# Kernel tuning notes

Measured on AMD Instinct MI355X. Metric: run time of the kernel, lower is better.

Reference implementation:

```python
import jax, jax.numpy as jnp
import numpy as np

COND_EPS = 1e-12  # singularity threshold for the 2x2 Hessian determinant


def setup_inputs() -> dict:
    key = jax.random.key(0)
    k1, k2 = jax.random.split(key)
    b, h, w = 8, 1024, 1536
    # neur_beta_eme: non-negative-ish network output (forward clamps at 0 anyway)
    neur_beta_eme = jax.random.uniform(k1, (b, 1, h, w), dtype=jnp.float32) * 2.0
    base_detector_score = jax.random.normal(k2, (b, 1, h, w), dtype=jnp.float32)
    return {
        "neur_beta_eme": neur_beta_eme,
        "base_detector_score": base_detector_score,
        "n": 2048,
        "border_size": 16,
    }


def _gather(score_flat, y, x, w):
    # score_flat: [b, h*w]; y,x: [b,n] -> [b,n]
    return jnp.take_along_axis(score_flat, y * w + x, axis=-1)


def reference(neur_beta_eme, base_detector_score, n, border_size):
    b, _, h, w = base_detector_score.shape
    # NeSSDetector.forward: model(image)[-1].clamp(min=0)
    neur = jnp.maximum(neur_beta_eme, 0.0)
    score = base_detector_score

    # base_detector.get_extrema_mask: 3x3 NMS (local max) + border exclusion
    pooled = jax.lax.reduce_window(score, -jnp.inf, jax.lax.max,
                                   (1, 1, 3, 3), (1, 1, 1, 1), "SAME")
    ys = jnp.arange(h)
    xs = jnp.arange(w)
    border = (((ys >= border_size) & (ys < h - border_size))[:, None]
              & ((xs >= border_size) & (xs < w - border_size))[None, :])
    extrema_mask = (score == pooled) & border[None, None]

    # ness_extrema_map = exp(-neur_beta_eme) * extrema_mask
    ness = jnp.exp(-neur) * extrema_mask.astype(score.dtype)

    # topk over flattened spatial dims
    ness_flat = ness.reshape(b, -1)                      # [b, h*w]
    _, flat_cand_kp = jax.lax.top_k(ness_flat, n)        # [b, n]

    # flat2grid(flat, w) + 0.5  (pixel-center coords, (y, x) order)
    y = flat_cand_kp // w
    x = flat_cand_kp % w
    cand_kp = jnp.stack([y, x], axis=-1).astype(score.dtype) + 0.5  # [b, n, 2]

    # localize_keypoints_via_taylor: 3x3 finite-difference gradient/Hessian,
    # solve H @ inc = -g per keypoint (2x2 closed-form solve)
    sf = score.reshape(b, -1)
    yc = jnp.clip(y, 1, h - 2)
    xc = jnp.clip(x, 1, w - 2)
    s00 = _gather(sf, yc, xc, w)
    sp0 = _gather(sf, yc + 1, xc, w)
    sm0 = _gather(sf, yc - 1, xc, w)
    s0p = _gather(sf, yc, xc + 1, w)
    s0m = _gather(sf, yc, xc - 1, w)
    spp = _gather(sf, yc + 1, xc + 1, w)
    spm = _gather(sf, yc + 1, xc - 1, w)
    smp = _gather(sf, yc - 1, xc + 1, w)
    smm = _gather(sf, yc - 1, xc - 1, w)

    gy = 0.5 * (sp0 - sm0)
    gx = 0.5 * (s0p - s0m)
    hyy = sp0 - 2.0 * s00 + sm0
    hxx = s0p - 2.0 * s00 + s0m
    hxy = 0.25 * (spp - spm - smp + smm)

    det = hyy * hxx - hxy * hxy
    sing_mask = jnp.abs(det) > COND_EPS
    safe_det = jnp.where(sing_mask, det, 1.0)
    inc_y = -(hxx * gy - hxy * gx) / safe_det
    inc_x = -(hyy * gx - hxy * gy) / safe_det
    inc = jnp.stack([inc_y, inc_x], axis=-1)             # [b, n, 2]
    inc = jnp.clip(jnp.where(sing_mask[..., None], inc, 0.0), -0.5, 0.5)

    kp = cand_kp + inc                                   # [b, n, 2]

    # kp_neur_beta_eme = neur.view(b,-1).gather(-1, flat_cand_kp)
    kp_neur = jnp.take_along_axis(neur.reshape(b, -1), flat_cand_kp, axis=-1)

    return jnp.concatenate([kp, kp_neur[..., None]], axis=-1)  # [b, n, 3]
```

## Files before the change

kernel.cpp:

```cpp
#include <hip/hip_runtime.h>
#include <math.h>

typedef unsigned int u32;
typedef unsigned long long u64;

#define B 8
#define H 1024
#define W 1536
#define NPIX (H * W)
#define NK 2048
#define BORDER 16
#define NSEG 64
#define TY 8
#define NTILE 6
#define GRIDY 31
#define HBINS 512
#define TOPK_CAP 4096
#define SEG_CAP_MAX 4096
#define CTR_PAD 32
#define IDX_MASK 0x1FFFFFu

#define OFF_TCOUNT 128
#define OFF_HIST   4096
#define OFF_SEGCNT 20480
#define OFF_RANK   86016
#define OFF_KEYS   217088
#define OFF_CAND   479232

__global__ __launch_bounds__(256) void cand_k(const float* __restrict__ neur,
                                              const float* __restrict__ score,
                                              u32* __restrict__ candp,
                                              u32* __restrict__ segcnt,
                                              u32* __restrict__ hist, int seg_cap) {
    __shared__ u32 lh[HBINS];
    int tile = blockIdx.x;
    int b = blockIdx.z;
    int wave = threadIdx.x >> 6;
    int lane = threadIdx.x & 63;
    for (int i = threadIdx.x; i < HBINS; i += 256) lh[i] = 0;
    __syncthreads();

    int strip = blockIdx.y * 4 + wave;
    int y0 = BORDER + strip * TY;
    int x0 = tile * 256 + lane * 4;
    const float* s = score + (size_t)b * NPIX;
    const float* nb = neur + (size_t)b * NPIX;
    bool haveL = (tile > 0) && (lane == 0);
    bool haveR = (tile < NTILE - 1) && (lane == 63);

    float4 rv[TY + 2];
    float4 nvv[TY];
    float le[TY + 2], re[TY + 2];
    const float* base_row = s + (size_t)(y0 - 1) * W + x0;
    const float* nrow = nb + (size_t)y0 * W + x0;
    #pragma unroll
    for (int r = 0; r < TY + 2; ++r) rv[r] = *(const float4*)(base_row + (size_t)r * W);
    #pragma unroll
    for (int r = 0; r < TY; ++r) nvv[r] = *(const float4*)(nrow + (size_t)r * W);
    #pragma unroll
    for (int r = 0; r < TY + 2; ++r) {
        le[r] = haveL ? base_row[(size_t)r * W - 1] : 0.0f;
        re[r] = haveR ? base_row[(size_t)r * W + 4] : 0.0f;
    }

    bool xok[4];
    #pragma unroll
    for (int e = 0; e < 4; ++e) {
        int x = x0 + e;
        xok[e] = (x >= BORDER) && (x < W - BORDER);
    }

    u32 extbits = 0;
    {
        float4 hm, h0, hp;
        #pragma unroll
        for (int r = 0; r < 2; ++r) {
            float4 c = rv[r];
            float l = __shfl_up(c.w, 1); if (haveL) l = le[r];
            float rr = __shfl_down(c.x, 1); if (haveR) rr = re[r];
            float4 hh;
            hh.x = fmaxf(fmaxf(l, c.x), c.y);
            hh.y = fmaxf(fmaxf(c.x, c.y), c.z);
            hh.z = fmaxf(fmaxf(c.y, c.z), c.w);
            hh.w = fmaxf(fmaxf(c.z, c.w), rr);
            if (r == 0) hm = hh; else h0 = hh;
        }
        #pragma unroll
        for (int ys = 0; ys < TY; ++ys) {
            float4 c = rv[ys + 2];
            float l = __shfl_up(c.w, 1); if (haveL) l = le[ys + 2];
            float rr = __shfl_down(c.x, 1); if (haveR) rr = re[ys + 2];
            hp.x = fmaxf(fmaxf(l, c.x), c.y);
            hp.y = fmaxf(fmaxf(c.x, c.y), c.z);
            hp.z = fmaxf(fmaxf(c.y, c.z), c.w);
            hp.w = fmaxf(fmaxf(c.z, c.w), rr);
            float pv[4];
            pv[0] = fmaxf(fmaxf(hm.x, h0.x), hp.x);
            pv[1] = fmaxf(fmaxf(hm.y, h0.y), hp.y);
            pv[2] = fmaxf(fmaxf(hm.z, h0.z), hp.z);
            pv[3] = fmaxf(fmaxf(hm.w, h0.w), hp.w);
            float4 c0 = rv[ys + 1];
            float cv[4] = {c0.x, c0.y, c0.z, c0.w};
            #pragma unroll
            for (int e = 0; e < 4; ++e)
                if (xok[e] && cv[e] >= pv[e]) extbits |= (1u << (ys * 4 + e));
            hm = h0; h0 = hp;
        }
    }

    u32 c = (u32)__popc(extbits);
    u32 scan = c;
    #pragma unroll
    for (int off = 1; off < 64; off <<= 1) {
        u32 o = (u32)__shfl_up((int)scan, off, 64);
        if (lane >= off) scan += o;
    }
    u32 excl = scan - c;
    u32 tot = (u32)__shfl((int)scan, 63, 64);
    if (tot) {
        int seg = (strip * NTILE + tile) & (NSEG - 1);
        u32* ctr = &segcnt[(u32)(b * NSEG + seg) * CTR_PAD];
        u32 base = 0;
        if (lane == 63) base = atomicAdd(ctr, scan);
        base = (u32)__shfl((int)base, 63, 64);
        u32 pos0 = base + excl;
        u32 sbase = (u32)(b * NSEG + seg) * (u32)seg_cap;
        u32 idxbase = (u32)(y0 * W + x0);
        #pragma unroll
        for (int k = 0; k < 32; ++k) {
            if (extbits & (1u << k)) {
                const int ro = k >> 2, e = k & 3;
                float4 nq = nvv[ro];
                float raw = (e == 0) ? nq.x : (e == 1) ? nq.y : (e == 2) ? nq.z : nq.w;
                float nv = fmaxf(raw, 0.0f);
                u32 fb = __float_as_uint(nv);
                u32 bin = fb >> 21; if (bin > HBINS - 1) bin = HBINS - 1;
                atomicAdd(&lh[bin], 1u);
                u32 idx = idxbase + (u32)ro * W + (u32)e;
                u32 p = pos0 + (u32)__popc(extbits & ((1u << k) - 1u));
                if ((int)p < seg_cap) candp[sbase + p] = (bin << 21) | idx;
            }
        }
    }
    __syncthreads();
    for (int i = threadIdx.x; i < HBINS; i += 256) {
        u32 v = lh[i];
        if (v) atomicAdd(&hist[(u32)b * HBINS + i], v);
    }
}

__global__ __launch_bounds__(256) void compact_k(const u32* __restrict__ candp,
                                                 const u32* __restrict__ segcnt,
                                                 const u32* __restrict__ hist,
                                                 const float* __restrict__ neur,
                                                 u64* __restrict__ keysout,
                                                 u32* tcount, int seg_cap) {
    __shared__ u32 piv_s;
    int seg = blockIdx.x;
    int b = blockIdx.y;
    int lane = threadIdx.x & 63;
    if (threadIdx.x < 64) {
        if (threadIdx.x == 0) piv_s = 0xFFFFFFFFu;
        u32 v[8];
        u32 s8 = 0;
        #pragma unroll
        for (int e = 0; e < 8; ++e) {
            v[e] = hist[(u32)b * HBINS + (u32)threadIdx.x * 8u + e];
            s8 += v[e];
        }
        u32 incl = s8;
        #pragma unroll
        for (int off = 1; off < 64; off <<= 1) {
            u32 o = (u32)__shfl_up((int)incl, off, 64);
            if (lane >= off) incl += o;
        }
        u32 excl = incl - s8;
        if (excl < NK && incl >= NK) {
            u32 cum = excl;
            u32 T = 0;
            #pragma unroll
            for (int e = 0; e < 8; ++e) {
                cum += v[e];
                if (cum >= NK) { T = (u32)threadIdx.x * 8u + e; break; }
            }
            piv_s = (T + 2u) << 21;
        }
    }
    __syncthreads();
    u32 piv = piv_s;
    const float* nb = neur + (size_t)b * NPIX;

    u32 cnt = segcnt[(u32)(b * NSEG + seg) * CTR_PAD];
    if ((int)cnt > seg_cap) cnt = (u32)seg_cap;
    u32 base = (u32)(b * NSEG + seg) * (u32)seg_cap;
    u32 iters = (cnt + 255u) / 256u;
    for (u32 it = 0; it < iters; ++it) {
        u32 i = it * 256u + threadIdx.x;
        bool f = false;
        u32 idx = 0;
        if (i < cnt) {
            u32 p = candp[base + i];
            f = (p < piv);
            idx = p & IDX_MASK;
        }
        u64 m = __ballot((int)f);
        if (m) {
            int leader = __ffsll((long long)m) - 1;
            u32 wbase = 0;
            if (lane == leader) wbase = atomicAdd(&tcount[b * CTR_PAD], (u32)__popcll(m));
            wbase = (u32)__shfl((int)wbase, leader, 64);
            if (f) {
                u32 pos = wbase + (u32)__popcll(m & ((1ull << (u32)lane) - 1ull));
                if (pos < TOPK_CAP) {
                    float nv = fmaxf(nb[idx], 0.0f);
                    float ness = (float)exp(-(double)nv);
                    keysout[(u32)b * TOPK_CAP + pos] =
                        ((u64)__float_as_uint(ness) << 32) | (u32)(~idx);
                }
            }
        }
    }
}

__global__ __launch_bounds__(1024) void rank_k(const u64* __restrict__ keys,
                                               u32* __restrict__ rank) {
    __shared__ u64 jk[1024];
    int b = blockIdx.z;
    u32 i = blockIdx.x * 1024u + threadIdx.x;
    u64 ki = keys[(u32)b * TOPK_CAP + i];
    jk[threadIdx.x] = keys[(u32)b * TOPK_CAP + blockIdx.y * 1024u + threadIdx.x];
    __syncthreads();
    u32 r = 0;
    #pragma unroll 8
    for (int j = 0; j < 1024; ++j) r += (jk[j] > ki) ? 1u : 0u;
    if (r) atomicAdd(&rank[(u32)b * TOPK_CAP + i], r);
}

__global__ __launch_bounds__(256) void refine_k(const float* __restrict__ neur,
                                                const float* __restrict__ score,
                                                const u64* __restrict__ keys,
                                                const u32* __restrict__ rank,
                                                float* __restrict__ out) {
    int b = blockIdx.y;
    u32 i = blockIdx.x * 256u + threadIdx.x;
    u32 r = rank[(u32)b * TOPK_CAP + i];
    if (r >= NK) return;
    const float* s = score + (size_t)b * NPIX;
    const float* nb = neur + (size_t)b * NPIX;
    u64 key = keys[(u32)b * TOPK_CAP + i];
    u32 idx = ~(u32)key;
    if (idx >= (u32)NPIX) return;
    int y = (int)(idx / W), x = (int)(idx % W);
    int yc = min(max(y, 1), H - 2), xc = min(max(x, 1), W - 2);
    int p = yc * W + xc;
    float s00 = s[p], sp0 = s[p + W], sm0 = s[p - W], s0p = s[p + 1], s0m = s[p - 1];
    float spp = s[p + W + 1], spm = s[p + W - 1], smp = s[p - W + 1], smm = s[p - W - 1];
    float gy = 0.5f * (sp0 - sm0);
    float gx = 0.5f * (s0p - s0m);
    float hyy = sp0 - 2.0f * s00 + sm0;
    float hxx = s0p - 2.0f * s00 + s0m;
    float hxy = 0.25f * (spp - spm - smp + smm);
    float det = hyy * hxx - hxy * hxy;
    bool sing = fabsf(det) > 1e-12f;
    float sd = sing ? det : 1.0f;
    float iy = -(hxx * gy - hxy * gx) / sd;
    float ix = -(hyy * gx - hxy * gy) / sd;
    if (!sing) { iy = 0.0f; ix = 0.0f; }
    iy = fminf(fmaxf(iy, -0.5f), 0.5f);
    ix = fminf(fmaxf(ix, -0.5f), 0.5f);
    size_t o = ((size_t)b * NK + (size_t)r) * 3;
    out[o] = (float)y + 0.5f + iy;
    out[o + 1] = (float)x + 0.5f + ix;
    out[o + 2] = fmaxf(nb[idx], 0.0f);
}

extern "C" void kernel_launch(void* const* d_in, const int* in_sizes, int n_in,
                              void* d_out, int out_size, void* d_ws, size_t ws_size,
                              hipStream_t stream) {
    const float* neur = (const float*)d_in[0];
    const float* score = (const float*)d_in[1];
    float* out = (float*)d_out;
    char* ws = (char*)d_ws;
    u32* tcount = (u32*)(ws + OFF_TCOUNT);
    u32* hist = (u32*)(ws + OFF_HIST);
    u32* segcnt = (u32*)(ws + OFF_SEGCNT);
    u32* rank = (u32*)(ws + OFF_RANK);
    u64* keysbuf = (u64*)(ws + OFF_KEYS);
    u32* candp = (u32*)(ws + OFF_CAND);

    size_t avail = ws_size > OFF_CAND ? ws_size - OFF_CAND : 0;
    long long cap_ll = (long long)(avail / (4ull * B * NSEG));
    int seg_cap = cap_ll > SEG_CAP_MAX ? SEG_CAP_MAX : (int)cap_ll;

    hipMemsetAsync(ws, 0, OFF_CAND, stream);
    cand_k<<<dim3(NTILE, GRIDY, B), 256, 0, stream>>>(neur, score, candp, segcnt, hist, seg_cap);
    compact_k<<<dim3(NSEG, B), 256, 0, stream>>>(candp, segcnt, hist, neur, keysbuf, tcount, seg_cap);
    rank_k<<<dim3(TOPK_CAP / 1024, TOPK_CAP / 1024, B), 1024, 0, stream>>>(keysbuf, rank);
    refine_k<<<dim3(TOPK_CAP / 256, B), 256, 0, stream>>>(neur, score, keysbuf, rank, out);
}
```

Before: 178.7 us.

## Fuse rank and refine kernels, load all keys to LDS, drop rank memset

Merges the separate rank-counting and refinement kernels into a single kernel. Each block loads the batch's full key array (masked by the valid count) into shared memory and computes each key's rank directly, so the global rank buffer, its atomics and part of the workspace memset are no longer needed. Removing one launch and the rank buffer traffic is the main aim. In exchange each block now scans 4096 keys instead of 1024, the grid shrinks from 128 blocks of 1024 threads to 128 blocks of 256 threads, and each block needs 32KB of LDS, which reduces parallelism for the rank computation.

```diff
diff --git a/kernel.cpp b/kernel.cpp
--- a/kernel.cpp
+++ b/kernel.cpp
@@ -23,9 +23,9 @@
 #define OFF_TCOUNT 128
 #define OFF_HIST   4096
 #define OFF_SEGCNT 20480
-#define OFF_RANK   86016
-#define OFF_KEYS   217088
-#define OFF_CAND   479232
+#define OFF_ZERO_END 86016
+#define OFF_KEYS   86016
+#define OFF_CAND   348160
 
 __global__ __launch_bounds__(256) void cand_k(const float* __restrict__ neur,
                                               const float* __restrict__ score,
@@ -222,34 +222,30 @@
     }
 }
 
-__global__ __launch_bounds__(1024) void rank_k(const u64* __restrict__ keys,
-                                               u32* __restrict__ rank) {
-    __shared__ u64 jk[1024];
-    int b = blockIdx.z;
-    u32 i = blockIdx.x * 1024u + threadIdx.x;
-    u64 ki = keys[(u32)b * TOPK_CAP + i];
-    jk[threadIdx.x] = keys[(u32)b * TOPK_CAP + blockIdx.y * 1024u + threadIdx.x];
-    __syncthreads();
+__global__ __launch_bounds__(256) void rankref_k(const float* __restrict__ neur,
+                                                 const float* __restrict__ score,
+                                                 const u64* __restrict__ keys,
+                                                 const u32* __restrict__ tcount,
+                                                 float* __restrict__ out) {
+    __shared__ u64 jk[TOPK_CAP];
+    int b = blockIdx.y;
+    u32 cnt = tcount[(u32)b * CTR_PAD];
+    if (cnt > TOPK_CAP) cnt = TOPK_CAP;
+    for (u32 t = threadIdx.x; t < TOPK_CAP; t += 256u)
+        jk[t] = (t < cnt) ? keys[(u32)b * TOPK_CAP + t] : 0ull;
+    __syncthreads();
+
+    u32 i = blockIdx.x * 256u + threadIdx.x;
+    u64 ki = jk[i];
     u32 r = 0;
-    #pragma unroll 8
-    for (int j = 0; j < 1024; ++j) r += (jk[j] > ki) ? 1u : 0u;
-    if (r) atomicAdd(&rank[(u32)b * TOPK_CAP + i], r);
-}
-
-__global__ __launch_bounds__(256) void refine_k(const float* __restrict__ neur,
-                                                const float* __restrict__ score,
-                                                const u64* __restrict__ keys,
-                                                const u32* __restrict__ rank,
-                                                float* __restrict__ out) {
-    int b = blockIdx.y;
-    u32 i = blockIdx.x * 256u + threadIdx.x;
-    u32 r = rank[(u32)b * TOPK_CAP + i];
-    if (r >= NK) return;
+    #pragma unroll 16
+    for (int j = 0; j < TOPK_CAP; ++j) r += (jk[j] > ki) ? 1u : 0u;
+    if (i >= cnt || r >= NK) return;
+
+    u32 idx = ~(u32)ki;
+    if (idx >= (u32)NPIX) return;
     const float* s = score + (size_t)b * NPIX;
     const float* nb = neur + (size_t)b * NPIX;
-    u64 key = keys[(u32)b * TOPK_CAP + i];
-    u32 idx = ~(u32)key;
-    if (idx >= (u32)NPIX) return;
     int y = (int)(idx / W), x = (int)(idx % W);
     int yc = min(max(y, 1), H - 2), xc = min(max(x, 1), W - 2);
     int p = yc * W + xc;
@@ -284,7 +280,6 @@
     u32* tcount = (u32*)(ws + OFF_TCOUNT);
     u32* hist = (u32*)(ws + OFF_HIST);
     u32* segcnt = (u32*)(ws + OFF_SEGCNT);
-    u32* rank = (u32*)(ws + OFF_RANK);
     u64* keysbuf = (u64*)(ws + OFF_KEYS);
     u32* candp = (u32*)(ws + OFF_CAND);
 
@@ -292,9 +287,8 @@
     long long cap_ll = (long long)(avail / (4ull * B * NSEG));
     int seg_cap = cap_ll > SEG_CAP_MAX ? SEG_CAP_MAX : (int)cap_ll;
 
-    hipMemsetAsync(ws, 0, OFF_CAND, stream);
+    hipMemsetAsync(ws, 0, OFF_ZERO_END, stream);
     cand_k<<<dim3(NTILE, GRIDY, B), 256, 0, stream>>>(neur, score, candp, segcnt, hist, seg_cap);
     compact_k<<<dim3(NSEG, B), 256, 0, stream>>>(candp, segcnt, hist, neur, keysbuf, tcount, seg_cap);
-    rank_k<<<dim3(TOPK_CAP / 1024, TOPK_CAP / 1024, B), 1024, 0, stream>>>(keysbuf, rank);
-    refine_k<<<dim3(TOPK_CAP / 256, B), 256, 0, stream>>>(neur, score, keysbuf, rank, out);
-}
+    rankref_k<<<dim3(TOPK_CAP / 256, B), 256, 0, stream>>>(neur, score, keysbuf, tcount, out);
+}
```

Result: slower. 201.3 us (+12.6%).
